# Performance work log

Hardware: AMD Instinct MI355X
Metric: run time of the kernel (lower is better)

## Reference

```python
import jax, jax.numpy as jnp
import numpy as np

WINDOW_SIZE = 2
SOFTMAX_TEMP = 0.01
EPS = 1e-12  # F.normalize default eps


def _l2_normalize(x, axis):
    n = jnp.sqrt(jnp.sum(x * x, axis=axis, keepdims=True))
    return x / jnp.maximum(n, EPS)


def setup_inputs() -> dict:
    key = jax.random.key(0)
    k1, k2, k3 = jax.random.split(key, 3)
    B, C, N = 16, 128, 4096
    return {
        "keypoint_coords": jax.random.normal(k1, (B, 2, N), dtype=jnp.float32),
        "keypoint_weights": jax.random.uniform(k2, (B, 1, N), dtype=jnp.float32),
        "keypoint_desc": jax.random.normal(k3, (B, C, N), dtype=jnp.float32),
    }


def reference(keypoint_coords, keypoint_weights, keypoint_desc):
    # split interleaved src/tgt frames along batch
    src_coords = keypoint_coords[::WINDOW_SIZE]    # [b,2,N]
    tgt_coords = keypoint_coords[1::WINDOW_SIZE]   # [b,2,M]
    src_weights = keypoint_weights[::WINDOW_SIZE]  # [b,1,N]
    tgt_weights = keypoint_weights[1::WINDOW_SIZE] # [b,1,M]
    src_desc = keypoint_desc[::WINDOW_SIZE]        # [b,C,N]
    tgt_desc = keypoint_desc[1::WINDOW_SIZE]       # [b,C,M]

    C = src_desc.shape[1]
    src_desc_norm = _l2_normalize(src_desc, axis=1)
    tgt_desc_norm = _l2_normalize(tgt_desc, axis=1)

    # cosine similarity matrix [b,N,M]
    match_vals = jnp.einsum("bcn,bcm->bnm", src_desc_norm, tgt_desc_norm)
    soft_match_vals = jax.nn.softmax(match_vals / SOFTMAX_TEMP, axis=2)

    # reuse the attention matrix for three value matmuls
    pseudo_coords = jnp.einsum("bcm,bnm->bcn", tgt_coords, soft_match_vals)   # [b,2,N]
    pseudo_desc = jnp.einsum("bcm,bnm->bcn", tgt_desc, soft_match_vals)       # [b,C,N]
    pseudo_desc = _l2_normalize(pseudo_desc, axis=1)
    pseudo_weights = jnp.einsum("bim,bnm->bin", tgt_weights, soft_match_vals) # [b,1,N]

    desc_match_score = jnp.sum(src_desc * pseudo_desc, axis=1, keepdims=True) / float(C)
    match_weights = 0.5 * (desc_match_score + 1.0) * src_weights * pseudo_weights
    return pseudo_coords, match_weights
```

## Files before the change

### kernel.cpp

```cpp
#include <hip/hip_runtime.h>
#include <math.h>

#define C 128
#define N 4096
#define BP 8
#define TN 64

typedef __attribute__((ext_vector_type(8))) short bf16x8;
typedef __attribute__((ext_vector_type(16))) float f32x16;
typedef __attribute__((ext_vector_type(4))) int i32x4;
typedef __attribute__((ext_vector_type(16))) int i32x16;

#define PREP_OFF 65536
#define FRAGS_PER_MT 18
#define SUBT_BYTES (FRAGS_PER_MT * 1024)
#define BLOB_BYTES ((size_t)BP * 128 * FRAGS_PER_MT * 1024)

__device__ __forceinline__ unsigned short bf16rnd(float x) {
  unsigned u = __float_as_uint(x);
  u += 0x7fffu + ((u >> 16) & 1u);
  return (unsigned short)(u >> 16);
}
__device__ __forceinline__ float bf16up(unsigned short h) {
  return __uint_as_float(((unsigned)h) << 16);
}
__device__ __forceinline__ int rne2(float x, float y) {
  unsigned ux = __float_as_uint(x); ux += 0x7fffu + ((ux >> 16) & 1u);
  unsigned uy = __float_as_uint(y); uy += 0x7fffu + ((uy >> 16) & 1u);
  return (int)__builtin_amdgcn_perm(uy, ux, 0x07060302u);
}
__device__ __forceinline__ int trunc2(float x, float y) {
  return (int)__builtin_amdgcn_perm(__float_as_uint(y), __float_as_uint(x), 0x07060302u);
}
__device__ __forceinline__ float truncres(float x) {
  return x - __uint_as_float(__float_as_uint(x) & 0xffff0000u);
}
__device__ __forceinline__ int pk4(int a, int b, int c, int d) {
  return (a & 255) | ((b & 255) << 8) | ((c & 255) << 16) | ((d & 255) << 24);
}

__global__ __launch_bounds__(256) void knorm_inv(const float* __restrict__ desc,
                                                 float* __restrict__ inv) {
  int n = blockIdx.x * 256 + threadIdx.x;
  int b = 2 * blockIdx.y + 1;
  const float* d = desc + (size_t)b * C * N + n;
  float ssq = 0.f;
#pragma unroll 8
  for (int c = 0; c < C; ++c) {
    float v = d[(size_t)c * N];
    ssq = fmaf(v, v, ssq);
  }
  inv[b * N + n] = 1.0f / fmaxf(sqrtf(ssq), 1e-12f);
}

__global__ __launch_bounds__(256) void kprep(
    const float* __restrict__ coords, const float* __restrict__ wtsp,
    const float* __restrict__ desc, unsigned char* __restrict__ blob) {
  const int mt = blockIdx.x;
  const int p = blockIdx.y;
  const int tb = 2 * p + 1;
  const int m0 = mt * 32;
  const int t = threadIdx.x;
  const int ks = t >> 6;
  const int h = (t >> 5) & 1;
  const int l31 = t & 31;

  __shared__ float rss[8][32];

  const float* tgtd = desc + (size_t)tb * C * N;
  unsigned char* bl = blob + ((size_t)(p * 128 + mt) * FRAGS_PER_MT) * 1024;

  float vr[16];
  float part = 0.f;
#pragma unroll
  for (int i = 0; i < 16; ++i) {
    float v = tgtd[(size_t)(32 * ks + 16 * h + i) * N + m0 + l31];
    vr[i] = v;
    part = fmaf(v, v, part);
  }
  rss[ks * 2 + h][l31] = part;
  __syncthreads();
  float ssq = 0.f;
#pragma unroll
  for (int u = 0; u < 8; ++u) ssq += rss[u][l31];
  const float invm = 1.0f / fmaxf(sqrtf(ssq), 1e-12f);

  {
    int hb[16], lb[16];
#pragma unroll
    for (int i = 0; i < 16; ++i) {
      int q = (int)rintf(vr[i] * invm * 16384.f);
      int hi = (q + 128) >> 8;
      hb[i] = hi;
      lb[i] = q - (hi << 8);
    }
    int4 ph = make_int4(pk4(hb[0], hb[1], hb[2], hb[3]), pk4(hb[4], hb[5], hb[6], hb[7]),
                        pk4(hb[8], hb[9], hb[10], hb[11]), pk4(hb[12], hb[13], hb[14], hb[15]));
    int4 pl = make_int4(pk4(lb[0], lb[1], lb[2], lb[3]), pk4(lb[4], lb[5], lb[6], lb[7]),
                        pk4(lb[8], lb[9], lb[10], lb[11]), pk4(lb[12], lb[13], lb[14], lb[15]));
    int lane = 32 * h + l31;
    *(int4*)(bl + (size_t)ks * 1024 + lane * 16) = ph;
    *(int4*)(bl + (size_t)(4 + ks) * 1024 + lane * 16) = pl;
  }

#pragma unroll
  for (int it = 0; it < 4; ++it) {
    int e = t + 256 * it;
    int c = e >> 3, mq = e & 7;
    float4 v = *(const float4*)&tgtd[(size_t)c * N + m0 + 4 * mq];
    int f = (c >> 5) * 2 + (mq >> 2);
    int slot = (c & 31) + 32 * ((mq >> 1) & 1);
    int2 pk;
    pk.x = rne2(v.x, v.y);
    pk.y = rne2(v.z, v.w);
    *(int2*)(bl + (size_t)(8 + f) * 1024 + slot * 16 + (mq & 1) * 8) = pk;
  }

  if (t < 128) {
    int fe = t >> 6, slot = t & 63, r = slot & 31, hh = slot >> 5;
    int4 pk = make_int4(0, 0, 0, 0);
    if (r < 4) {
      const float* rp = (r == 0)   ? coords + (size_t)tb * 2 * N
                        : (r == 1) ? coords + (size_t)tb * 2 * N + N
                                   : wtsp + (size_t)tb * N;
      int mb = m0 + 16 * fe + 8 * hh;
      float v[8];
#pragma unroll
      for (int i = 0; i < 8; ++i) v[i] = (r == 3) ? 1.0f : rp[mb + i];
      pk.x = rne2(v[0], v[1]);
      pk.y = rne2(v[2], v[3]);
      pk.z = rne2(v[4], v[5]);
      pk.w = rne2(v[6], v[7]);
    }
    *(int4*)(bl + (size_t)(16 + fe) * 1024 + slot * 16) = pk;
  }
}

#define LDS_SHORTS 20480

__global__ __launch_bounds__(256, 2) void kmain(
    const float* __restrict__ wtsp, const float* __restrict__ desc,
    const unsigned char* __restrict__ blob, float* __restrict__ out) {
  const int bid = blockIdx.x;
  const int p = bid & 7;
  const int ntile = bid >> 3;
  const int sb = 2 * p;
  const int n0 = ntile * TN;
  const int tid = threadIdx.x;
  const int w = tid >> 6;
  const int ln = tid & 63;
  const int l31 = ln & 31;
  const int h = ln >> 5;
  const int wn = w & 1;
  const int st = w >> 1;

  __shared__ __align__(16) short L[LDS_SHORTS];

  const float* srcd = desc + (size_t)sb * C * N;
  const unsigned char* wblob = blob + (size_t)p * 128 * SUBT_BYTES;
  const int nn = n0 + 32 * wn + l31;

  float ssq = 0.f;
#pragma unroll
  for (int ks = 0; ks < 4; ++ks) {
#pragma unroll
    for (int i = 0; i < 16; ++i) {
      float v = srcd[(size_t)(32 * ks + 16 * h + i) * N + nn];
      ssq = fmaf(v, v, ssq);
    }
  }
  ssq += __shfl_xor(ssq, 32);
  const float invs = 1.0f / fmaxf(sqrtf(ssq), 1e-12f);

  i32x4 Qhi[4], Qlo[4];
#pragma unroll
  for (int ks = 0; ks < 4; ++ks) {
    int hb[16], lb[16];
#pragma unroll
    for (int i = 0; i < 16; ++i) {
      float v = srcd[(size_t)(32 * ks + 16 * h + i) * N + nn] * invs;
      int q = (int)rintf(v * 16384.f);
      int hi = (q + 128) >> 8;
      hb[i] = hi;
      lb[i] = q - (hi << 8);
    }
    i32x4 qh = {pk4(hb[0], hb[1], hb[2], hb[3]), pk4(hb[4], hb[5], hb[6], hb[7]),
                pk4(hb[8], hb[9], hb[10], hb[11]), pk4(hb[12], hb[13], hb[14], hb[15])};
    i32x4 ql = {pk4(lb[0], lb[1], lb[2], lb[3]), pk4(lb[4], lb[5], lb[6], lb[7]),
                pk4(lb[8], lb[9], lb[10], lb[11]), pk4(lb[12], lb[13], lb[14], lb[15])};
    Qhi[ks] = qh;
    Qlo[ks] = ql;
  }

  f32x16 acc[5];
#pragma unroll
  for (int t = 0; t < 5; ++t)
#pragma unroll
    for (int r = 0; r < 16; ++r) acc[t][r] = 0.f;

  i32x16 zz;
#pragma unroll
  for (int r = 0; r < 16; ++r) zz[r] = 0;

  auto issue_dma = [&](int it2, int bufb) {
    const unsigned char* s0 = wblob + (size_t)(it2 * 2) * SUBT_BYTES + ln * 16;
#pragma unroll
    for (int jj = 0; jj < 4; ++jj) {
      int jg = 4 * w + jj;
      const unsigned char* src = s0 + (size_t)(jg >> 3) * SUBT_BYTES + (size_t)(jg & 7) * 1024;
      __builtin_amdgcn_global_load_lds(
          (const void __attribute__((address_space(1)))*)src,
          (void __attribute__((address_space(3)))*)&L[bufb * 8192 + jg * 512], 16, 0, 0);
    }
  };
  auto loadV = [&](int it2, int s2, bf16x8* V) {
    const unsigned char* vb =
        wblob + (size_t)(it2 * 2 + st) * SUBT_BYTES + (size_t)(8 + s2) * 1024 + ln * 16;
#pragma unroll
    for (int t = 0; t < 5; ++t) V[t] = *(const bf16x8*)(vb + (size_t)(2 * t) * 1024);
  };

  issue_dma(0, 0);
  bf16x8 V0[5], V1[5];
  loadV(0, 0, V0);
  __syncthreads();

  for (int it = 0; it < 64; ++it) {
    const int cb = it & 1;
    if (it < 63) issue_dma(it + 1, cb ^ 1);

    const short* vb = &L[cb * 8192 + st * 4096];

    i32x16 Shh, Sx;
    {
      i32x4 ah = *(const i32x4*)&vb[0 * 512 + ln * 8];
      i32x4 al = *(const i32x4*)&vb[4 * 512 + ln * 8];
      Shh = __builtin_amdgcn_mfma_i32_32x32x32_i8(ah, Qhi[0], zz, 0, 0, 0);
      Sx = __builtin_amdgcn_mfma_i32_32x32x32_i8(ah, Qlo[0], zz, 0, 0, 0);
      Sx = __builtin_amdgcn_mfma_i32_32x32x32_i8(al, Qhi[0], Sx, 0, 0, 0);
    }
#pragma unroll
    for (int ks = 1; ks < 4; ++ks) {
      i32x4 ah = *(const i32x4*)&vb[ks * 512 + ln * 8];
      i32x4 al = *(const i32x4*)&vb[(4 + ks) * 512 + ln * 8];
      Shh = __builtin_amdgcn_mfma_i32_32x32x32_i8(ah, Qhi[ks], Shh, 0, 0, 0);
      Sx = __builtin_amdgcn_mfma_i32_32x32x32_i8(ah, Qlo[ks], Sx, 0, 0, 0);
      Sx = __builtin_amdgcn_mfma_i32_32x32x32_i8(al, Qhi[ks], Sx, 0, 0, 0);
    }

    loadV(it, 1, V1);

    int pp[8], xpp[8];
#pragma unroll
    for (int q = 0; q < 4; ++q) {
      float pv[4];
#pragma unroll
      for (int j = 0; j < 4; ++j) {
        int r = 4 * q + j;
        int tot = (Shh[r] << 8) + Sx[r];
        pv[j] = __expf(fmaf((float)tot, 9.5367431640625e-5f, -60.0f));
      }
      pp[2 * q] = rne2(pv[0], pv[1]);
      pp[2 * q + 1] = rne2(pv[2], pv[3]);
    }
#pragma unroll
    for (int j = 0; j < 8; ++j) xpp[j] = __shfl_xor(pp[j], 32);

    {
      int4 bi;
      if (h == 0)
        bi = make_int4(pp[0], pp[1], xpp[0], xpp[1]);
      else
        bi = make_int4(xpp[2], xpp[3], pp[2], pp[3]);
      bf16x8 bh = __builtin_bit_cast(bf16x8, bi);
#pragma unroll
      for (int t = 0; t < 5; ++t)
        acc[t] = __builtin_amdgcn_mfma_f32_32x32x16_bf16(V0[t], bh, acc[t], 0, 0, 0);
    }

    {
      int itn = (it < 63) ? it + 1 : 63;
      loadV(itn, 0, V0);
    }

    {
      int4 bi;
      if (h == 0)
        bi = make_int4(pp[4], pp[5], xpp[4], xpp[5]);
      else
        bi = make_int4(xpp[6], xpp[7], pp[6], pp[7]);
      bf16x8 bh = __builtin_bit_cast(bf16x8, bi);
#pragma unroll
      for (int t = 0; t < 5; ++t)
        acc[t] = __builtin_amdgcn_mfma_f32_32x32x16_bf16(V1[t], bh, acc[t], 0, 0, 0);
    }

    __syncthreads();
  }

  float* red = (float*)&L[0];
  if (st == 1) {
#pragma unroll
    for (int t = 0; t < 5; ++t)
#pragma unroll
      for (int r = 0; r < 16; ++r)
        red[wn * 5120 + t * 1024 + r * 64 + ln] = acc[t][r];
  }
  __syncthreads();

  if (st == 0) {
#pragma unroll
    for (int t = 0; t < 5; ++t)
#pragma unroll
      for (int r = 0; r < 16; ++r)
        acc[t][r] += red[wn * 5120 + t * 1024 + r * 64 + ln];

    float ssqd = 0.f, dotr = 0.f;
#pragma unroll
    for (int t = 0; t < 4; ++t) {
#pragma unroll
      for (int r = 0; r < 16; ++r) {
        int c = 32 * t + (r & 3) + 8 * (r >> 2) + 4 * h;
        float d = acc[t][r];
        ssqd = fmaf(d, d, ssqd);
        dotr = fmaf(d, srcd[(size_t)c * N + nn], dotr);
      }
    }
    ssqd += __shfl_xor(ssqd, 32);
    dotr += __shfl_xor(dotr, 32);
    if (h == 0) {
      float x = acc[4][0], y = acc[4][1], wv = acc[4][2], Ld = acc[4][3];
      float invL = 1.0f / Ld;
      float nrm = fmaxf(sqrtf(ssqd), 1e-30f);
      float score = dotr / (nrm * 128.0f);
      float sw = wtsp[(size_t)sb * N + nn];
      out[(size_t)p * 2 * N + nn] = x * invL;
      out[(size_t)p * 2 * N + N + nn] = y * invL;
      out[(size_t)(BP * 2 * N) + (size_t)p * N + nn] =
          0.5f * (score + 1.0f) * sw * wv * invL;
    }
  }
}

#define OFF_VMH3 0
#define OFF_VML3 8192
#define OFF_VCM3 16384
#define OFF_PH3 26624
#define LDS3_SHORTS 30720

__global__ __launch_bounds__(256, 2) void kmain_v3(
    const float* __restrict__ coords, const float* __restrict__ wtsp,
    const float* __restrict__ desc, const float* __restrict__ inv,
    float* __restrict__ out) {
  const int ntile = blockIdx.x;
  const int p = blockIdx.y;
  const int sb = 2 * p, tb = 2 * p + 1;
  const int n0 = ntile * TN;
  const int tid = threadIdx.x;
  const int w = tid >> 6;
  const int ln = tid & 63;
  const int l31 = ln & 31;
  const int h = ln >> 5;
  const int wn = w & 1;
  const int st = w >> 1;
  const int pt = wn * 64 + ln;

  __shared__ __align__(16) short L[LDS3_SHORTS];

  const float* srcd = desc + (size_t)sb * C * N;
  const float* tgtd = desc + (size_t)tb * C * N;
  const float* invtg = inv + tb * N;
  const float* tcx = coords + (size_t)tb * 2 * N;
  const float* tcy = tcx + N;
  const float* twp = wtsp + (size_t)tb * N;
  const int nn = n0 + 32 * wn + l31;

  float ssq = 0.f;
#pragma unroll
  for (int k = 0; k < 8; ++k) {
    int cb = 16 * k + 8 * h;
#pragma unroll
    for (int i = 0; i < 8; ++i) {
      float v = srcd[(size_t)(cb + i) * N + nn];
      ssq = fmaf(v, v, ssq);
    }
  }
  ssq += __shfl_xor(ssq, 32);
  float invs = 1.0f / fmaxf(sqrtf(ssq), 1e-12f);

  bf16x8 Qh[8], Ql[8];
#pragma unroll
  for (int k = 0; k < 8; ++k) {
    int cb = 16 * k + 8 * h;
    bf16x8 qh, ql;
#pragma unroll
    for (int i = 0; i < 8; ++i) {
      float v = srcd[(size_t)(cb + i) * N + nn] * invs;
      unsigned short hs = bf16rnd(v);
      unsigned short ls = bf16rnd(v - bf16up(hs));
      qh[i] = (short)hs;
      ql[i] = (short)ls;
    }
    Qh[k] = qh;
    Ql[k] = ql;
  }

  {
    int* z = (int*)&L[OFF_VCM3];
    for (int i = tid; i < 1024; i += 256) {
      int sI = i >> 9, j = i & 511;
      z[sI * 2560 + 2048 + j] = 0;
    }
  }

  f32x16 acc[5];
#pragma unroll
  for (int t = 0; t < 5; ++t)
#pragma unroll
    for (int r = 0; r < 16; ++r) acc[t][r] = 0.f;

  const int er = pt & 3, ehh = (pt >> 2) & 1, esf = pt >> 3;
  const float* erp = (er == 0) ? tcx : (er == 1) ? tcy : twp;

  float vm[32];
  float invm = 0.f;
  float4 exv0 = make_float4(1, 1, 1, 1), exv1 = exv0;

  auto prefetch = [&](int ms0) {
#pragma unroll
    for (int k = 0; k < 4; ++k) {
      int cb = 16 * (2 * k + wn) + 8 * h;
#pragma unroll
      for (int i = 0; i < 8; ++i)
        vm[k * 8 + i] = tgtd[(size_t)(cb + i) * N + ms0 + l31];
    }
    invm = invtg[ms0 + l31];
    if (pt < 16 && er < 3) {
      int mb = ms0 + 16 * esf + 8 * ehh;
      exv0 = *(const float4*)&erp[mb];
      exv1 = *(const float4*)&erp[mb + 4];
    }
  };

  prefetch(32 * st);

  for (int m0 = 0; m0 < N; m0 += 64) {
    const int ms0 = m0 + 32 * st;
    float4 vc[8];
#pragma unroll
    for (int it = 0; it < 8; ++it) {
      int e = pt + 128 * it, c = e >> 3, mq = e & 7;
      vc[it] = *(const float4*)&tgtd[(size_t)c * N + ms0 + 4 * mq];
    }
#pragma unroll
    for (int k = 0; k < 4; ++k) {
      int kk = 2 * k + wn;
      int hw[4], lw[4];
#pragma unroll
      for (int j = 0; j < 4; ++j) {
        float v0 = vm[k * 8 + 2 * j] * invm;
        float v1 = vm[k * 8 + 2 * j + 1] * invm;
        hw[j] = trunc2(v0, v1);
        lw[j] = trunc2(truncres(v0), truncres(v1));
      }
      *(int4*)&L[OFF_VMH3 + st * 4096 + kk * 512 + ln * 8] =
          make_int4(hw[0], hw[1], hw[2], hw[3]);
      *(int4*)&L[OFF_VML3 + st * 4096 + kk * 512 + ln * 8] =
          make_int4(lw[0], lw[1], lw[2], lw[3]);
    }
#pragma unroll
    for (int it = 0; it < 8; ++it) {
      int e = pt + 128 * it, c = e >> 3, mq = e & 7;
      float4 v = vc[it];
      int f = (c >> 5) * 2 + (mq >> 2);
      int slot = (c & 31) + 32 * ((mq >> 1) & 1);
      int2 pk;
      pk.x = rne2(v.x, v.y);
      pk.y = rne2(v.z, v.w);
      *(int2*)&L[OFF_VCM3 + st * 5120 + f * 512 + slot * 8 + (mq & 1) * 4] = pk;
    }
    if (pt < 16) {
      int4 pk;
      pk.x = rne2(exv0.x, exv0.y);
      pk.y = rne2(exv0.z, exv0.w);
      pk.z = rne2(exv1.x, exv1.y);
      pk.w = rne2(exv1.z, exv1.w);
      *(int4*)&L[OFF_VCM3 + st * 5120 + (8 + esf) * 512 + (er + 32 * ehh) * 8] = pk;
    }
    __syncthreads();
    if (m0 + 64 < N) prefetch(ms0 + 64);

    f32x16 S;
#pragma unroll
    for (int r = 0; r < 16; ++r) S[r] = 0.f;
    const short* vmh = &L[OFF_VMH3 + st * 4096];
    const short* vml = &L[OFF_VML3 + st * 4096];
#pragma unroll
    for (int k = 0; k < 8; ++k) {
      bf16x8 ah = *(const bf16x8*)&vmh[k * 512 + ln * 8];
      bf16x8 al = *(const bf16x8*)&vml[k * 512 + ln * 8];
      S = __builtin_amdgcn_mfma_f32_32x32x16_bf16(al, Qh[k], S, 0, 0, 0);
      S = __builtin_amdgcn_mfma_f32_32x32x16_bf16(ah, Ql[k], S, 0, 0, 0);
      S = __builtin_amdgcn_mfma_f32_32x32x16_bf16(ah, Qh[k], S, 0, 0, 0);
    }
#pragma unroll
    for (int q = 0; q < 4; ++q) {
      float p0 = __expf(fmaf(S[4 * q + 0], 100.0f, -60.0f));
      float p1 = __expf(fmaf(S[4 * q + 1], 100.0f, -60.0f));
      float p2 = __expf(fmaf(S[4 * q + 2], 100.0f, -60.0f));
      float p3 = __expf(fmaf(S[4 * q + 3], 100.0f, -60.0f));
      int2 a;
      a.x = rne2(p0, p1);
      a.y = rne2(p2, p3);
      *(int2*)&L[OFF_PH3 + w * 1024 + (q >> 1) * 512 + (l31 + 32 * (q & 1)) * 8 + h * 4] = a;
    }
#pragma unroll
    for (int s2 = 0; s2 < 2; ++s2) {
      bf16x8 bh = *(const bf16x8*)&L[OFF_PH3 + w * 1024 + s2 * 512 + ln * 8];
#pragma unroll
      for (int t = 0; t < 5; ++t) {
        bf16x8 va = *(const bf16x8*)&L[OFF_VCM3 + st * 5120 + (2 * t + s2) * 512 + ln * 8];
        acc[t] = __builtin_amdgcn_mfma_f32_32x32x16_bf16(va, bh, acc[t], 0, 0, 0);
      }
    }
    __syncthreads();
  }

  float* red = (float*)&L[0];
  if (st == 1) {
#pragma unroll
    for (int t = 0; t < 5; ++t)
#pragma unroll
      for (int r = 0; r < 16; ++r)
        red[wn * 5120 + t * 1024 + r * 64 + ln] = acc[t][r];
  }
  __syncthreads();
  if (st == 0) {
#pragma unroll
    for (int t = 0; t < 5; ++t)
#pragma unroll
      for (int r = 0; r < 16; ++r)
        acc[t][r] += red[wn * 5120 + t * 1024 + r * 64 + ln];
    float ssqd = 0.f, dotr = 0.f;
#pragma unroll
    for (int t = 0; t < 4; ++t) {
#pragma unroll
      for (int r = 0; r < 16; ++r) {
        int c = 32 * t + (r & 3) + 8 * (r >> 2) + 4 * h;
        float d = acc[t][r];
        ssqd = fmaf(d, d, ssqd);
        dotr = fmaf(d, srcd[(size_t)c * N + nn], dotr);
      }
    }
    ssqd += __shfl_xor(ssqd, 32);
    dotr += __shfl_xor(dotr, 32);
    if (h == 0) {
      float x = acc[4][0], y = acc[4][1], wv = acc[4][2], Ld = acc[4][3];
      float invL = 1.0f / Ld;
      float nrm = fmaxf(sqrtf(ssqd), 1e-30f);
      float score = dotr / (nrm * 128.0f);
      float sw = wtsp[(size_t)sb * N + nn];
      out[(size_t)p * 2 * N + nn] = x * invL;
      out[(size_t)p * 2 * N + N + nn] = y * invL;
      out[(size_t)(BP * 2 * N) + (size_t)p * N + nn] =
          0.5f * (score + 1.0f) * sw * wv * invL;
    }
  }
}

extern "C" void kernel_launch(void* const* d_in, const int* in_sizes, int n_in,
                              void* d_out, int out_size, void* d_ws, size_t ws_size,
                              hipStream_t stream) {
  const float* coords = (const float*)d_in[0];
  const float* wts = (const float*)d_in[1];
  const float* desc = (const float*)d_in[2];
  float* out = (float*)d_out;
  float* inv = (float*)d_ws;
  unsigned char* blob = (unsigned char*)d_ws + PREP_OFF;

  if (ws_size >= PREP_OFF + BLOB_BYTES) {
    kprep<<<dim3(128, BP), 256, 0, stream>>>(coords, wts, desc, blob);
    kmain<<<dim3((N / TN) * BP), 256, 0, stream>>>(wts, desc, blob, out);
  } else {
    knorm_inv<<<dim3(N / 256, BP), 256, 0, stream>>>(desc, inv);
    kmain_v3<<<dim3(N / TN, BP), 256, 0, stream>>>(coords, wts, desc, inv, out);
  }
}
```

Before: 185.2 us.

## Quad-buffer LDS tiles with two iterations per barrier and add low-low int8 term

```diff
diff --git a/kernel.cpp b/kernel.cpp
--- a/kernel.cpp
+++ b/kernel.cpp
@@ -136,7 +136,7 @@
   }
 }
 
-#define LDS_SHORTS 20480
+#define LDS_SHORTS 32768
 
 __global__ __launch_bounds__(256, 2) void kmain(
     const float* __restrict__ wtsp, const float* __restrict__ desc,
@@ -202,15 +202,16 @@
 #pragma unroll
   for (int r = 0; r < 16; ++r) zz[r] = 0;
 
-  auto issue_dma = [&](int it2, int bufb) {
-    const unsigned char* s0 = wblob + (size_t)(it2 * 2) * SUBT_BYTES + ln * 16;
+  auto issue_dma = [&](int it) {
+    const unsigned char* s0 = wblob + (size_t)(it * 2) * SUBT_BYTES + ln * 16;
+    short* dst = &L[(it & 3) * 8192];
 #pragma unroll
     for (int jj = 0; jj < 4; ++jj) {
       int jg = 4 * w + jj;
       const unsigned char* src = s0 + (size_t)(jg >> 3) * SUBT_BYTES + (size_t)(jg & 7) * 1024;
       __builtin_amdgcn_global_load_lds(
           (const void __attribute__((address_space(1)))*)src,
-          (void __attribute__((address_space(3)))*)&L[bufb * 8192 + jg * 512], 16, 0, 0);
+          (void __attribute__((address_space(3)))*)&dst[jg * 512], 16, 0, 0);
     }
   };
   auto loadV = [&](int it2, int s2, bf16x8* V) {
@@ -220,23 +221,18 @@
     for (int t = 0; t < 5; ++t) V[t] = *(const bf16x8*)(vb + (size_t)(2 * t) * 1024);
   };
 
-  issue_dma(0, 0);
   bf16x8 V0[5], V1[5];
-  loadV(0, 0, V0);
-  __syncthreads();
-
-  for (int it = 0; it < 64; ++it) {
-    const int cb = it & 1;
-    if (it < 63) issue_dma(it + 1, cb ^ 1);
-
-    const short* vb = &L[cb * 8192 + st * 4096];
-
-    i32x16 Shh, Sx;
+
+  auto compute_iter = [&](int it) {
+    const short* vb = &L[(it & 3) * 8192 + st * 4096];
+
+    i32x16 Shh, Sx, Sll;
     {
       i32x4 ah = *(const i32x4*)&vb[0 * 512 + ln * 8];
       i32x4 al = *(const i32x4*)&vb[4 * 512 + ln * 8];
       Shh = __builtin_amdgcn_mfma_i32_32x32x32_i8(ah, Qhi[0], zz, 0, 0, 0);
       Sx = __builtin_amdgcn_mfma_i32_32x32x32_i8(ah, Qlo[0], zz, 0, 0, 0);
+      Sll = __builtin_amdgcn_mfma_i32_32x32x32_i8(al, Qlo[0], zz, 0, 0, 0);
       Sx = __builtin_amdgcn_mfma_i32_32x32x32_i8(al, Qhi[0], Sx, 0, 0, 0);
     }
 #pragma unroll
@@ -245,6 +241,7 @@
       i32x4 al = *(const i32x4*)&vb[(4 + ks) * 512 + ln * 8];
       Shh = __builtin_amdgcn_mfma_i32_32x32x32_i8(ah, Qhi[ks], Shh, 0, 0, 0);
       Sx = __builtin_amdgcn_mfma_i32_32x32x32_i8(ah, Qlo[ks], Sx, 0, 0, 0);
+      Sll = __builtin_amdgcn_mfma_i32_32x32x32_i8(al, Qlo[ks], Sll, 0, 0, 0);
       Sx = __builtin_amdgcn_mfma_i32_32x32x32_i8(al, Qhi[ks], Sx, 0, 0, 0);
     }
 
@@ -258,7 +255,8 @@
       for (int j = 0; j < 4; ++j) {
         int r = 4 * q + j;
         int tot = (Shh[r] << 8) + Sx[r];
-        pv[j] = __expf(fmaf((float)tot, 9.5367431640625e-5f, -60.0f));
+        float sf = fmaf((float)tot, 256.f, (float)Sll[r]);
+        pv[j] = __expf(fmaf(sf, 3.7252903e-07f, -60.0f));
       }
       pp[2 * q] = rne2(pv[0], pv[1]);
       pp[2 * q + 1] = rne2(pv[2], pv[3]);
@@ -294,7 +292,20 @@
       for (int t = 0; t < 5; ++t)
         acc[t] = __builtin_amdgcn_mfma_f32_32x32x16_bf16(V1[t], bh, acc[t], 0, 0, 0);
     }
-
+  };
+
+  issue_dma(0);
+  issue_dma(1);
+  loadV(0, 0, V0);
+  __syncthreads();
+
+  for (int it2 = 0; it2 < 32; ++it2) {
+    if (it2 < 31) {
+      issue_dma(2 * it2 + 2);
+      issue_dma(2 * it2 + 3);
+    }
+    compute_iter(2 * it2);
+    compute_iter(2 * it2 + 1);
     __syncthreads();
   }
 
```

New measurement: 203.4 us. 9.8% more time.
